# Optimization experiments

Hardware: AMD Instinct MI355X
Metric: run time of the kernel (lower is better)

Reference implementation:

```python
import jax, jax.numpy as jnp
import numpy as np

B, T, EMB, HS = 512, 256, 364, 64

def setup_inputs() -> dict:
    key = jax.random.key(0)
    ks = jax.random.split(key, 7)
    s = EMB ** -0.5  # keep weight scale sane
    return {
        "x": jax.random.normal(ks[0], (B, T, EMB), jnp.float32),
        "Wk": jax.random.normal(ks[1], (EMB, HS), jnp.float32) * s,
        "bk": jax.random.normal(ks[2], (HS,), jnp.float32) * 0.01,
        "Wq": jax.random.normal(ks[3], (EMB, HS), jnp.float32) * s,
        "bq": jax.random.normal(ks[4], (HS,), jnp.float32) * 0.01,
        "Wv": jax.random.normal(ks[5], (EMB, HS), jnp.float32) * s,
        "bv": jax.random.normal(ks[6], (HS,), jnp.float32) * 0.01,
    }

def reference(x, Wk, bk, Wq, bq, Wv, bv):
    # Faithful to the original: wei = k @ q^T (note swapped q/k vs textbook),
    # scaled by head_size**-0.5, causal mask, softmax, (dropout = identity in eval), then @ v.
    k = x @ Wk + bk          # [B, T, HS]
    q = x @ Wq + bq          # [B, T, HS]
    v = x @ Wv + bv          # [B, T, HS]
    scale = k.shape[-1] ** -0.5
    wei = jnp.einsum('btd,bsd->bts', k, q) * scale  # [B, T, T]
    causal = jnp.tril(jnp.ones((T, T), dtype=bool))
    wei = jnp.where(causal, wei, -jnp.inf)
    wei = jax.nn.softmax(wei, axis=-1)
    out = jnp.einsum('bts,bsd->btd', wei, v)        # [B, T, HS]
    return out
```

## Files before the change

kernel.cpp:

```cpp
#include <hip/hip_runtime.h>
#include <math.h>

#define BB   512
#define TT   256
#define EMBD 364
#define HS   64
#define KPAD 384
#define NC   192
#define LP   72

typedef __attribute__((ext_vector_type(8))) short short8_t;
typedef __attribute__((ext_vector_type(4))) float f32x4;

__device__ __forceinline__ ushort f2bf(float v) {
    union { float f; unsigned u; } c; c.f = v;
    unsigned b = c.u;
    return (ushort)((b + 0x7FFF + ((b >> 16) & 1)) >> 16);
}

#define WT_BYTES  ((size_t)NC * KPAD * 2)
#define KQ_ELEMS  ((size_t)BB * TT * HS)
#define K_OFF_B   (WT_BYTES)
#define Q_OFF_B   (K_OFF_B + KQ_ELEMS * 2)
#define VT_OFF_B  (Q_OFF_B + KQ_ELEMS * 2)
#define WS_NEEDED (VT_OFF_B + KQ_ELEMS * 2)

__global__ void prep_wt(const float* __restrict__ Wk, const float* __restrict__ Wq,
                        const float* __restrict__ Wv, ushort* __restrict__ WT)
{
    const int c = blockIdx.x;
    const float* Wp = (c < 64) ? Wk : (c < 128 ? Wq : Wv);
    const float s  = (c < 64) ? 0.125f : 1.0f;
    const int col  = c & 63;
    for (int e = threadIdx.x; e < KPAD; e += 64) {
        float v = (e < EMBD) ? Wp[(size_t)e * HS + col] * s : 0.f;
        WT[(size_t)c * KPAD + e] = f2bf(v);
    }
}

__global__ __launch_bounds__(256, 4) void proj_gemm(
    const float* __restrict__ x, const ushort* __restrict__ WT,
    const float* __restrict__ bk_, const float* __restrict__ bq_,
    const float* __restrict__ bv_,
    ushort* __restrict__ Kg, ushort* __restrict__ Qg, ushort* __restrict__ Vt)
{
    const int blk = blockIdx.x;
    const int tid = threadIdx.x;
    const int l   = tid & 63;
    const int w   = tid >> 6;
    const int l15 = l & 15;
    const int lg  = l >> 4;

    __shared__ ushort xs[2][64 * LP];

    const float* xb = x + (size_t)blk * 64 * EMBD;
    const int srow = tid >> 2;
    const int scol = (tid & 3) * 16;

    float sreg[16];

    auto LOAD = [&](int kc) {
        const int k0 = kc * 64;
        if (kc < 5) {
            #pragma unroll
            for (int u = 0; u < 4; ++u) {
                float4 f = *(const float4*)&xb[(size_t)srow * EMBD + k0 + scol + u * 4];
                sreg[u * 4 + 0] = f.x; sreg[u * 4 + 1] = f.y;
                sreg[u * 4 + 2] = f.z; sreg[u * 4 + 3] = f.w;
            }
        } else {
            #pragma unroll
            for (int u = 0; u < 16; ++u) {
                int k = k0 + scol + u;
                sreg[u] = (k < EMBD) ? xb[(size_t)srow * EMBD + k] : 0.f;
            }
        }
    };
    auto WRITE = [&](int buf) {
        union { short8_t s8; ushort u[8]; } p0, p1;
        #pragma unroll
        for (int u = 0; u < 8; ++u) { p0.u[u] = f2bf(sreg[u]); p1.u[u] = f2bf(sreg[8 + u]); }
        *(short8_t*)&xs[buf][srow * LP + scol]     = p0.s8;
        *(short8_t*)&xs[buf][srow * LP + scol + 8] = p1.s8;
    };

    f32x4 acc[4][3];
    #pragma unroll
    for (int mi = 0; mi < 4; ++mi)
        #pragma unroll
        for (int j = 0; j < 3; ++j) acc[mi][j] = (f32x4){0.f, 0.f, 0.f, 0.f};

    LOAD(0); WRITE(0);
    __syncthreads();

    for (int kc = 0; kc < 6; ++kc) {
        if (kc < 5) LOAD(kc + 1);
        const int buf = kc & 1;
        #pragma unroll
        for (int ks = 0; ks < 2; ++ks) {
            short8_t a[4];
            #pragma unroll
            for (int mi = 0; mi < 4; ++mi)
                a[mi] = *(const short8_t*)&xs[buf][(mi * 16 + l15) * LP + ks * 32 + lg * 8];
            #pragma unroll
            for (int j = 0; j < 3; ++j) {
                const int c = w * 48 + j * 16 + l15;
                short8_t bf = *(const short8_t*)&WT[(size_t)c * KPAD + kc * 64 + ks * 32 + lg * 8];
                #pragma unroll
                for (int mi = 0; mi < 4; ++mi)
                    acc[mi][j] = __builtin_amdgcn_mfma_f32_16x16x32_bf16(a[mi], bf, acc[mi][j], 0, 0, 0);
            }
        }
        if (kc < 5) WRITE(1 - buf);
        __syncthreads();
    }

    const int b   = blk >> 2;
    const int tl0 = (blk & 3) * 64;
    #pragma unroll
    for (int j = 0; j < 3; ++j) {
        const int c = w * 48 + j * 16 + l15;
        const float bias = (c < 64) ? bk_[c] * 0.125f
                         : (c < 128 ? bq_[c - 64] : bv_[c - 128]);
        #pragma unroll
        for (int mi = 0; mi < 4; ++mi) {
            const size_t trow = (size_t)blk * 64 + mi * 16 + lg * 4;
            if (c < 64) {
                #pragma unroll
                for (int r = 0; r < 4; ++r)
                    Kg[(trow + r) * HS + c] = f2bf(acc[mi][j][r] + bias);
            } else if (c < 128) {
                #pragma unroll
                for (int r = 0; r < 4; ++r)
                    Qg[(trow + r) * HS + (c - 64)] = f2bf(acc[mi][j][r] + bias);
            } else {
                ushort4 pk;
                pk.x = f2bf(acc[mi][j][0] + bias);
                pk.y = f2bf(acc[mi][j][1] + bias);
                pk.z = f2bf(acc[mi][j][2] + bias);
                pk.w = f2bf(acc[mi][j][3] + bias);
                const int tloc = tl0 + mi * 16 + lg * 4;
                *(ushort4*)&Vt[((size_t)b * HS + (c - 128)) * TT + tloc] = pk;
            }
        }
    }
}

__global__ __launch_bounds__(512, 4) void attn_fused(
    const ushort* __restrict__ Kg, const ushort* __restrict__ Qg,
    const ushort* __restrict__ Vt, float* __restrict__ out)
{
    const int b   = blockIdx.x;
    const int tid = threadIdx.x;
    const int l   = tid & 63;
    const int w   = tid >> 6;
    const int l15 = l & 15;
    const int lg  = l >> 4;

    __shared__ ushort pb[8][16 * 40];
    ushort* pbw = pb[w];

    const ushort* Kb = Kg + (size_t)b * TT * HS;
    const ushort* Qb = Qg + (size_t)b * TT * HS;
    const ushort* Vb = Vt + (size_t)b * HS * TT;

    #pragma unroll
    for (int half = 0; half < 2; ++half) {
        const int rt = half ? (15 - w) : w;
        const int t0 = rt * 16;

        short8_t afr[2];
        afr[0] = *(const short8_t*)&Kb[(t0 + l15) * HS + lg * 8];
        afr[1] = *(const short8_t*)&Kb[(t0 + l15) * HS + 32 + lg * 8];

        float mr[4], lr[4];
        f32x4 o[4];
        #pragma unroll
        for (int r = 0; r < 4; ++r) { mr[r] = -INFINITY; lr[r] = 0.f; }
        #pragma unroll
        for (int nt = 0; nt < 4; ++nt) o[nt] = (f32x4){0.f, 0.f, 0.f, 0.f};

        const int jd = t0 >> 5;
        for (int j = 0; j <= jd; ++j) {
            const int sb = j * 32;
            f32x4 sacc[2];
            sacc[0] = (f32x4){0.f, 0.f, 0.f, 0.f};
            sacc[1] = (f32x4){0.f, 0.f, 0.f, 0.f};
            #pragma unroll
            for (int kk = 0; kk < 2; ++kk) {
                #pragma unroll
                for (int ct = 0; ct < 2; ++ct) {
                    short8_t bfr = *(const short8_t*)&Qb[(sb + ct * 16 + l15) * HS + kk * 32 + lg * 8];
                    sacc[ct] = __builtin_amdgcn_mfma_f32_16x16x32_bf16(afr[kk], bfr, sacc[ct], 0, 0, 0);
                }
            }
            #pragma unroll
            for (int ct = 0; ct < 2; ++ct) {
                int s = sb + ct * 16 + l15;
                #pragma unroll
                for (int r = 0; r < 4; ++r) {
                    int t = t0 + lg * 4 + r;
                    if (s > t) sacc[ct][r] = -INFINITY;
                }
            }
            float p0[4], p1[4], fsc[4];
            #pragma unroll
            for (int r = 0; r < 4; ++r) {
                float mx = fmaxf(sacc[0][r], sacc[1][r]);
                mx = fmaxf(mx, __shfl_xor(mx, 1));
                mx = fmaxf(mx, __shfl_xor(mx, 2));
                mx = fmaxf(mx, __shfl_xor(mx, 4));
                mx = fmaxf(mx, __shfl_xor(mx, 8));
                float nm = fmaxf(mr[r], mx);
                fsc[r] = __expf(mr[r] - nm);
                mr[r] = nm;
                p0[r] = __expf(sacc[0][r] - nm);
                p1[r] = __expf(sacc[1][r] - nm);
                float ps = p0[r] + p1[r];
                ps += __shfl_xor(ps, 1);
                ps += __shfl_xor(ps, 2);
                ps += __shfl_xor(ps, 4);
                ps += __shfl_xor(ps, 8);
                lr[r] = lr[r] * fsc[r] + ps;
            }
            #pragma unroll
            for (int nt = 0; nt < 4; ++nt)
                #pragma unroll
                for (int r = 0; r < 4; ++r) o[nt][r] *= fsc[r];
            #pragma unroll
            for (int r = 0; r < 4; ++r) {
                pbw[(lg * 4 + r) * 40 + l15]      = f2bf(p0[r]);
                pbw[(lg * 4 + r) * 40 + 16 + l15] = f2bf(p1[r]);
            }
            short8_t pa = *(const short8_t*)&pbw[l15 * 40 + lg * 8];
            #pragma unroll
            for (int nt = 0; nt < 4; ++nt) {
                short8_t bfr = *(const short8_t*)&Vb[(nt * 16 + l15) * TT + sb + lg * 8];
                o[nt] = __builtin_amdgcn_mfma_f32_16x16x32_bf16(pa, bfr, o[nt], 0, 0, 0);
            }
        }
        #pragma unroll
        for (int r = 0; r < 4; ++r) {
            float inv = 1.0f / lr[r];
            int t = t0 + lg * 4 + r;
            float* op = out + ((size_t)b * TT + t) * HS;
            #pragma unroll
            for (int nt = 0; nt < 4; ++nt)
                op[nt * 16 + l15] = o[nt][r] * inv;
        }
    }
}

extern "C" void kernel_launch(void* const* d_in, const int* in_sizes, int n_in,
                              void* d_out, int out_size, void* d_ws, size_t ws_size,
                              hipStream_t stream) {
    const float* x  = (const float*)d_in[0];
    const float* Wk = (const float*)d_in[1];
    const float* bk = (const float*)d_in[2];
    const float* Wq = (const float*)d_in[3];
    const float* bq = (const float*)d_in[4];
    const float* Wv = (const float*)d_in[5];
    const float* bv = (const float*)d_in[6];
    float* out = (float*)d_out;

    ushort* WT = (ushort*)d_ws;
    ushort* Kg = (ushort*)((char*)d_ws + K_OFF_B);
    ushort* Qg = (ushort*)((char*)d_ws + Q_OFF_B);
    ushort* Vt = (ushort*)((char*)d_ws + VT_OFF_B);

    prep_wt<<<dim3(NC), dim3(64), 0, stream>>>(Wk, Wq, Wv, WT);
    proj_gemm<<<dim3(2048), dim3(256), 0, stream>>>(x, WT, bk, bq, bv, Kg, Qg, Vt);
    attn_fused<<<dim3(BB), dim3(512), 0, stream>>>(Kg, Qg, Vt, out);
}
```

Measured before the change: 128.0 us.

## Keep projection weights register-resident and stream x per-wave without block barriers

The weight matrix is pre-swizzled into MFMA fragment order so each wave loads its full B operand (3x12 fragments) into registers once, instead of re-reading WT from global memory every k-step. Each wave now stages its own 16-row slab of x in a private LDS tile and walks the four row tiles sequentially, with no __syncthreads. The tail chunk is loaded with float4 accesses instead of scalar guarded loads. The large register footprint lowers the launch bound to 2 blocks per CU, which cuts occupancy, and the x data per block is re-read in a more serialized order.

```diff
diff --git a/kernel.cpp b/kernel.cpp
--- a/kernel.cpp
+++ b/kernel.cpp
@@ -7,7 +7,6 @@
 #define HS   64
 #define KPAD 384
 #define NC   192
-#define LP   72
 
 typedef __attribute__((ext_vector_type(8))) short short8_t;
 typedef __attribute__((ext_vector_type(4))) float f32x4;
@@ -18,28 +17,33 @@
     return (ushort)((b + 0x7FFF + ((b >> 16) & 1)) >> 16);
 }
 
-#define WT_BYTES  ((size_t)NC * KPAD * 2)
+#define WTR_BYTES ((size_t)144 * 512 * 2)
 #define KQ_ELEMS  ((size_t)BB * TT * HS)
-#define K_OFF_B   (WT_BYTES)
+#define K_OFF_B   (WTR_BYTES)
 #define Q_OFF_B   (K_OFF_B + KQ_ELEMS * 2)
 #define VT_OFF_B  (Q_OFF_B + KQ_ELEMS * 2)
-#define WS_NEEDED (VT_OFF_B + KQ_ELEMS * 2)
-
-__global__ void prep_wt(const float* __restrict__ Wk, const float* __restrict__ Wq,
-                        const float* __restrict__ Wv, ushort* __restrict__ WT)
+
+__global__ void prep_wtr(const float* __restrict__ Wk, const float* __restrict__ Wq,
+                         const float* __restrict__ Wv, ushort* __restrict__ WTr)
 {
-    const int c = blockIdx.x;
+    const int bid = blockIdx.x;
+    const int jj  = bid / 12;
+    const int t   = bid % 12;
+    const int l   = threadIdx.x;
+    const int c   = jj * 16 + (l & 15);
     const float* Wp = (c < 64) ? Wk : (c < 128 ? Wq : Wv);
-    const float s  = (c < 64) ? 0.125f : 1.0f;
-    const int col  = c & 63;
-    for (int e = threadIdx.x; e < KPAD; e += 64) {
-        float v = (e < EMBD) ? Wp[(size_t)e * HS + col] * s : 0.f;
-        WT[(size_t)c * KPAD + e] = f2bf(v);
-    }
-}
-
-__global__ __launch_bounds__(256, 4) void proj_gemm(
-    const float* __restrict__ x, const ushort* __restrict__ WT,
+    const float s   = (c < 64) ? 0.125f : 1.0f;
+    const int col   = c & 63;
+    #pragma unroll
+    for (int i = 0; i < 8; ++i) {
+        int k = t * 32 + (l >> 4) * 8 + i;
+        float v = (k < EMBD) ? Wp[(size_t)k * HS + col] * s : 0.f;
+        WTr[((size_t)bid * 64 + l) * 8 + i] = f2bf(v);
+    }
+}
+
+__global__ __launch_bounds__(256, 2) void proj_gemm(
+    const float* __restrict__ x, const ushort* __restrict__ WTr,
     const float* __restrict__ bk_, const float* __restrict__ bq_,
     const float* __restrict__ bv_,
     ushort* __restrict__ Kg, ushort* __restrict__ Qg, ushort* __restrict__ Vt)
@@ -50,97 +54,112 @@
     const int w   = tid >> 6;
     const int l15 = l & 15;
     const int lg  = l >> 4;
-
-    __shared__ ushort xs[2][64 * LP];
+    const int srow = l >> 2;
+    const int scg  = l & 3;
+
+    __shared__ ushort xs_all[4][16 * 72];
+    ushort* xs = xs_all[w];
 
     const float* xb = x + (size_t)blk * 64 * EMBD;
-    const int srow = tid >> 2;
-    const int scol = (tid & 3) * 16;
-
-    float sreg[16];
-
-    auto LOAD = [&](int kc) {
-        const int k0 = kc * 64;
+
+    short8_t Bf[3][12];
+    #pragma unroll
+    for (int j = 0; j < 3; ++j)
+        #pragma unroll
+        for (int t = 0; t < 12; ++t)
+            Bf[j][t] = *(const short8_t*)&WTr[(((size_t)(w * 3 + j) * 12 + t) * 64 + l) * 8];
+
+    float bias3[3];
+    #pragma unroll
+    for (int j = 0; j < 3; ++j) {
+        int c = w * 48 + j * 16 + l15;
+        bias3[j] = (c < 64) ? bk_[c] * 0.125f : (c < 128 ? bq_[c - 64] : bv_[c - 128]);
+    }
+
+    float sA[16], sB[16];
+
+    auto LOADC = [&](int mt, int kc, float* s) {
+        const float* base = &xb[(size_t)(mt * 16 + srow) * EMBD + kc * 64 + scg * 16];
         if (kc < 5) {
             #pragma unroll
             for (int u = 0; u < 4; ++u) {
-                float4 f = *(const float4*)&xb[(size_t)srow * EMBD + k0 + scol + u * 4];
-                sreg[u * 4 + 0] = f.x; sreg[u * 4 + 1] = f.y;
-                sreg[u * 4 + 2] = f.z; sreg[u * 4 + 3] = f.w;
+                float4 f = *(const float4*)(base + u * 4);
+                s[u * 4 + 0] = f.x; s[u * 4 + 1] = f.y;
+                s[u * 4 + 2] = f.z; s[u * 4 + 3] = f.w;
             }
         } else {
-            #pragma unroll
-            for (int u = 0; u < 16; ++u) {
-                int k = k0 + scol + u;
-                sreg[u] = (k < EMBD) ? xb[(size_t)srow * EMBD + k] : 0.f;
+            if (scg < 2) {
+                #pragma unroll
+                for (int u = 0; u < 4; ++u) {
+                    float4 f = *(const float4*)(base + u * 4);
+                    s[u * 4 + 0] = f.x; s[u * 4 + 1] = f.y;
+                    s[u * 4 + 2] = f.z; s[u * 4 + 3] = f.w;
+                }
+            } else if (scg == 2) {
+                #pragma unroll
+                for (int u = 0; u < 3; ++u) {
+                    float4 f = *(const float4*)(base + u * 4);
+                    s[u * 4 + 0] = f.x; s[u * 4 + 1] = f.y;
+                    s[u * 4 + 2] = f.z; s[u * 4 + 3] = f.w;
+                }
+                #pragma unroll
+                for (int u = 12; u < 16; ++u) s[u] = 0.f;
+            } else {
+                #pragma unroll
+                for (int u = 0; u < 16; ++u) s[u] = 0.f;
             }
         }
     };
-    auto WRITE = [&](int buf) {
+    auto WRITEC = [&](const float* s) {
         union { short8_t s8; ushort u[8]; } p0, p1;
         #pragma unroll
-        for (int u = 0; u < 8; ++u) { p0.u[u] = f2bf(sreg[u]); p1.u[u] = f2bf(sreg[8 + u]); }
-        *(short8_t*)&xs[buf][srow * LP + scol]     = p0.s8;
-        *(short8_t*)&xs[buf][srow * LP + scol + 8] = p1.s8;
+        for (int u = 0; u < 8; ++u) { p0.u[u] = f2bf(s[u]); p1.u[u] = f2bf(s[8 + u]); }
+        *(short8_t*)&xs[srow * 72 + scg * 16]     = p0.s8;
+        *(short8_t*)&xs[srow * 72 + scg * 16 + 8] = p1.s8;
     };
 
-    f32x4 acc[4][3];
-    #pragma unroll
-    for (int mi = 0; mi < 4; ++mi)
-        #pragma unroll
-        for (int j = 0; j < 3; ++j) acc[mi][j] = (f32x4){0.f, 0.f, 0.f, 0.f};
-
-    LOAD(0); WRITE(0);
-    __syncthreads();
-
-    for (int kc = 0; kc < 6; ++kc) {
-        if (kc < 5) LOAD(kc + 1);
-        const int buf = kc & 1;
-        #pragma unroll
-        for (int ks = 0; ks < 2; ++ks) {
-            short8_t a[4];
-            #pragma unroll
-            for (int mi = 0; mi < 4; ++mi)
-                a[mi] = *(const short8_t*)&xs[buf][(mi * 16 + l15) * LP + ks * 32 + lg * 8];
+    LOADC(0, 0, sA);
+    LOADC(0, 1, sB);
+
+    for (int mt = 0; mt < 4; ++mt) {
+        f32x4 acc[3];
+        #pragma unroll
+        for (int j = 0; j < 3; ++j) acc[j] = (f32x4){0.f, 0.f, 0.f, 0.f};
+
+        #pragma unroll
+        for (int kc = 0; kc < 6; ++kc) {
+            float* cur = (kc & 1) ? sB : sA;
+            WRITEC(cur);
+            if (kc < 4)      LOADC(mt, kc + 2, cur);
+            else if (mt < 3) LOADC(mt + 1, kc - 4, cur);
+            short8_t a0 = *(const short8_t*)&xs[l15 * 72 + 0  + lg * 8];
+            short8_t a1 = *(const short8_t*)&xs[l15 * 72 + 32 + lg * 8];
             #pragma unroll
             for (int j = 0; j < 3; ++j) {
-                const int c = w * 48 + j * 16 + l15;
-                short8_t bf = *(const short8_t*)&WT[(size_t)c * KPAD + kc * 64 + ks * 32 + lg * 8];
-                #pragma unroll
-                for (int mi = 0; mi < 4; ++mi)
-                    acc[mi][j] = __builtin_amdgcn_mfma_f32_16x16x32_bf16(a[mi], bf, acc[mi][j], 0, 0, 0);
-            }
-        }
-        if (kc < 5) WRITE(1 - buf);
-        __syncthreads();
-    }
-
-    const int b   = blk >> 2;
-    const int tl0 = (blk & 3) * 64;
-    #pragma unroll
-    for (int j = 0; j < 3; ++j) {
-        const int c = w * 48 + j * 16 + l15;
-        const float bias = (c < 64) ? bk_[c] * 0.125f
-                         : (c < 128 ? bq_[c - 64] : bv_[c - 128]);
-        #pragma unroll
-        for (int mi = 0; mi < 4; ++mi) {
-            const size_t trow = (size_t)blk * 64 + mi * 16 + lg * 4;
-            if (c < 64) {
-                #pragma unroll
-                for (int r = 0; r < 4; ++r)
-                    Kg[(trow + r) * HS + c] = f2bf(acc[mi][j][r] + bias);
-            } else if (c < 128) {
-                #pragma unroll
-                for (int r = 0; r < 4; ++r)
-                    Qg[(trow + r) * HS + (c - 64)] = f2bf(acc[mi][j][r] + bias);
-            } else {
+                acc[j] = __builtin_amdgcn_mfma_f32_16x16x32_bf16(a0, Bf[j][kc * 2],     acc[j], 0, 0, 0);
+                acc[j] = __builtin_amdgcn_mfma_f32_16x16x32_bf16(a1, Bf[j][kc * 2 + 1], acc[j], 0, 0, 0);
+            }
+        }
+
+        const int b   = blk >> 2;
+        const int tl0 = (blk & 3) * 64 + mt * 16;
+        #pragma unroll
+        for (int j = 0; j < 3; ++j) {
+            const int c = w * 48 + j * 16 + l15;
+            #pragma unroll
+            for (int r = 0; r < 4; ++r) {
+                const size_t trow = (size_t)blk * 64 + mt * 16 + lg * 4 + r;
+                float val = acc[j][r] + bias3[j];
+                if (c < 64)       Kg[trow * HS + c]          = f2bf(val);
+                else if (c < 128) Qg[trow * HS + (c - 64)]   = f2bf(val);
+            }
+            if (c >= 128) {
                 ushort4 pk;
-                pk.x = f2bf(acc[mi][j][0] + bias);
-                pk.y = f2bf(acc[mi][j][1] + bias);
-                pk.z = f2bf(acc[mi][j][2] + bias);
-                pk.w = f2bf(acc[mi][j][3] + bias);
-                const int tloc = tl0 + mi * 16 + lg * 4;
-                *(ushort4*)&Vt[((size_t)b * HS + (c - 128)) * TT + tloc] = pk;
+                pk.x = f2bf(acc[j][0] + bias3[j]);
+                pk.y = f2bf(acc[j][1] + bias3[j]);
+                pk.z = f2bf(acc[j][2] + bias3[j]);
+                pk.w = f2bf(acc[j][3] + bias3[j]);
+                *(ushort4*)&Vt[((size_t)b * HS + (c - 128)) * TT + tl0 + lg * 4] = pk;
             }
         }
     }
@@ -263,12 +282,12 @@
     const float* bv = (const float*)d_in[6];
     float* out = (float*)d_out;
 
-    ushort* WT = (ushort*)d_ws;
-    ushort* Kg = (ushort*)((char*)d_ws + K_OFF_B);
-    ushort* Qg = (ushort*)((char*)d_ws + Q_OFF_B);
-    ushort* Vt = (ushort*)((char*)d_ws + VT_OFF_B);
-
-    prep_wt<<<dim3(NC), dim3(64), 0, stream>>>(Wk, Wq, Wv, WT);
-    proj_gemm<<<dim3(2048), dim3(256), 0, stream>>>(x, WT, bk, bq, bv, Kg, Qg, Vt);
+    ushort* WTr = (ushort*)d_ws;
+    ushort* Kg  = (ushort*)((char*)d_ws + K_OFF_B);
+    ushort* Qg  = (ushort*)((char*)d_ws + Q_OFF_B);
+    ushort* Vt  = (ushort*)((char*)d_ws + VT_OFF_B);
+
+    prep_wtr<<<dim3(144), dim3(64), 0, stream>>>(Wk, Wq, Wv, WTr);
+    proj_gemm<<<dim3(2048), dim3(256), 0, stream>>>(x, WTr, bk, bq, bv, Kg, Qg, Vt);
     attn_fused<<<dim3(BB), dim3(512), 0, stream>>>(Kg, Qg, Vt, out);
 }
```

Result: slower. 136.9 us (+6.9%).
